# Optimization experiments

Hardware: AMD Instinct MI355X
Metric: run time of the kernel (lower is better)

Reference implementation:

```python
import jax, jax.numpy as jnp
import numpy as np

H, W, NF, K, MD, ND, NDM, MLP_H = 128, 128, 8, 9, 16, 8, 8, 64
NPIX = H * W
RADIUS = int((K ** 0.5 - 1) // 2)


def _compute_neighbors_adjusted(height, width, radius):
    # Faithful port of LocalResiduals._compute_neighbors_adjusted (setup-time only).
    Kn = (2 * radius + 1) ** 2
    base = np.stack(np.meshgrid(np.arange(-radius, radius + 1),
                                np.arange(-radius, radius + 1), indexing='ij'),
                    axis=-1).reshape(-1, 2)
    neighbors = np.empty((height * width, Kn), dtype=np.int64)
    for i in range(height):
        for j in range(width):
            off = base.copy()
            ni = i + off[:, 0]
            nj = j + off[:, 1]
            valid = (ni >= 0) & (ni < height) & (nj >= 0) & (nj < width)
            valid_inds = list(ni[valid] * width + nj[valid])
            expansion = 1
            while len(valid_inds) < Kn:
                r_ext = radius + expansion
                ext = np.stack(np.meshgrid(np.arange(-r_ext, r_ext + 1),
                                           np.arange(-r_ext, r_ext + 1), indexing='ij'),
                               axis=-1).reshape(-1, 2)
                seen = set(map(tuple, off.tolist()))
                ext_new = np.array([t for t in map(tuple, ext.tolist()) if t not in seen],
                                   dtype=np.int64)
                off = np.concatenate([off, ext_new], axis=0)
                ni_e = i + ext_new[:, 0]
                nj_e = j + ext_new[:, 1]
                valid_e = (ni_e >= 0) & (ni_e < height) & (nj_e >= 0) & (nj_e < width)
                valid_inds += list(ni_e[valid_e] * width + nj_e[valid_e])
                expansion += 1
            neighbors[i * width + j] = np.array(valid_inds[:Kn], dtype=np.int64)
    return neighbors


def setup_inputs() -> dict:
    key = jax.random.key(0)
    ks = jax.random.split(key, 8)
    B = 16
    y_in = jax.random.normal(ks[0], (B, NF, H, W), dtype=jnp.float32)
    noise = jax.random.normal(ks[1], (B, ND, NPIX), dtype=jnp.float32)
    noise2 = jax.random.normal(ks[2], (B, NPIX, NDM), dtype=jnp.float32)
    n_in = NF + ND
    # xavier-uniform-like init for weight_map
    bound = float(np.sqrt(6.0 / (MD + n_in)))
    weight_map = jax.random.uniform(ks[3], (NPIX, K, MD, n_in), dtype=jnp.float32,
                                    minval=-bound, maxval=bound)
    d0 = MD + NDM
    w1 = jax.random.normal(ks[4], (MLP_H, d0), dtype=jnp.float32) / np.sqrt(d0)
    b1 = jnp.zeros((MLP_H,), dtype=jnp.float32)
    w2 = jax.random.normal(ks[5], (NF, MLP_H), dtype=jnp.float32) / np.sqrt(MLP_H)
    b2 = jnp.zeros((NF,), dtype=jnp.float32)
    neighbor_idx = jnp.asarray(_compute_neighbors_adjusted(H, W, RADIUS))  # (NPIX, K)
    return {"y_in": y_in, "noise": noise, "noise2": noise2,
            "weight_map": weight_map, "w1": w1, "b1": b1, "w2": w2, "b2": b2,
            "neighbor_idx": neighbor_idx}


def reference(y_in, noise, noise2, weight_map, w1, b1, w2, b2, neighbor_idx):
    B = y_in.shape[0]
    y_flat = y_in.reshape(B, NF, NPIX)
    y_with_noise = jnp.concatenate([y_flat, noise], axis=1)        # (B, NF+ND, NPIX)
    feats = jnp.transpose(y_with_noise, (0, 2, 1))                  # (B, NPIX, NF+ND)
    gather_y = feats[:, neighbor_idx, :]                            # (B, NPIX, K, NF+ND)
    # per-pixel distinct weight contraction
    intermediate = jnp.einsum('bpkn,pkmn->bpm', gather_y, weight_map)  # (B, NPIX, MD)
    mlp_in = jnp.concatenate([intermediate, noise2], axis=-1)      # (B, NPIX, MD+NDM)
    h = jax.nn.relu(jnp.einsum('bpd,hd->bph', mlp_in, w1) + b1)
    out = jnp.einsum('bph,fh->bpf', h, w2) + b2                    # (B, NPIX, NF)
    out = jnp.transpose(out, (0, 2, 1)).reshape(B, NF, H, W)
    return out
```

## Files before the change

### kernel.cpp

```cpp
#include <hip/hip_runtime.h>

#define NPIX 16384

typedef _Float16 f16;
typedef __attribute__((ext_vector_type(8))) _Float16 half8;
typedef __attribute__((ext_vector_type(8))) unsigned short ushort8;
typedef __attribute__((ext_vector_type(4))) float f32x4;

__device__ inline half8 cvt8_nt(const float* __restrict__ p) {
  f32x4 a = __builtin_nontemporal_load((const f32x4*)p);
  f32x4 b = __builtin_nontemporal_load((const f32x4*)p + 1);
  half8 r;
  r[0] = (f16)a.x; r[1] = (f16)a.y; r[2] = (f16)a.z; r[3] = (f16)a.w;
  r[4] = (f16)b.x; r[5] = (f16)b.y; r[6] = (f16)b.z; r[7] = (f16)b.w;
  return r;
}
__device__ inline half8 cvt8(const float* __restrict__ p) {
  f32x4 a = *(const f32x4*)p;
  f32x4 b = *(const f32x4*)(p + 4);
  half8 r;
  r[0] = (f16)a.x; r[1] = (f16)a.y; r[2] = (f16)a.z; r[3] = (f16)a.w;
  r[4] = (f16)b.x; r[5] = (f16)b.y; r[6] = (f16)b.z; r[7] = (f16)b.w;
  return r;
}

__global__ __launch_bounds__(256) void pack_feats(
    const float* __restrict__ y,
    const float* __restrict__ nz,
    f16* __restrict__ out)
{
  __shared__ f16 tile[64][258];
  const int p0 = blockIdx.x << 6;
  const int t = threadIdx.x;
  const int lane16 = t & 15;
  const int pl0 = t >> 4;
  #pragma unroll
  for (int g = 0; g < 16; ++g) {
    const int plane = g * 16 + pl0;
    const int b = plane >> 4, n = plane & 15;
    const float* src = (n < 8) ? (y + (b * 8 + n) * NPIX)
                               : (nz + (b * 8 + (n - 8)) * NPIX);
    f32x4 v = __builtin_nontemporal_load((const f32x4*)(src + p0 + lane16 * 4));
    tile[lane16 * 4 + 0][plane] = (f16)v.x;
    tile[lane16 * 4 + 1][plane] = (f16)v.y;
    tile[lane16 * 4 + 2][plane] = (f16)v.z;
    tile[lane16 * 4 + 3][plane] = (f16)v.w;
  }
  __syncthreads();
  #pragma unroll
  for (int it = 0; it < 8; ++it) {
    const int idx = it * 256 + t;
    const int px = idx >> 5;
    const int c = idx & 31;
    ushort8 v = *(const ushort8*)&tile[px][c * 8];
    *(ushort8*)(out + (p0 + px) * 256 + c * 8) = v;
  }
}

__global__ __launch_bounds__(256, 4) void lr_einsum(
    const f16*  __restrict__ feats,
    const float* __restrict__ wmap,
    const int*  __restrict__ nidx,
    f16* __restrict__ inter)
{
  const int t = threadIdx.x;
  const int wv = t >> 6;
  const int l = t & 63;
  const int col = l & 15;
  const int q = l >> 4;

  const int bid = blockIdx.x;
  const int p = ((((bid & 7) << 9) + (bid >> 3)) << 2) + wv;

  const int n0 = (q & 1) * 8;
  const int kh = q >> 1;

  const int ps = __builtin_amdgcn_readfirstlane(p);
  int nb[9];
  #pragma unroll
  for (int k = 0; k < 9; ++k)
    nb[k] = __builtin_amdgcn_readfirstlane(nidx[ps * 9 + k]);

  half8 af[5], bfr[5];
  #pragma unroll
  for (int c = 0; c < 4; ++c) {
    const int k = 2 * c + kh;
    af[c]  = *(const half8*)(feats + nb[k] * 256 + col * 16 + n0);
    bfr[c] = cvt8_nt(wmap + ((ps * 9 + k) * 16 + col) * 16 + n0);
  }
  af[4]  = (half8){0, 0, 0, 0, 0, 0, 0, 0};
  bfr[4] = (half8){0, 0, 0, 0, 0, 0, 0, 0};
  if (q < 2) {
    af[4]  = *(const half8*)(feats + nb[8] * 256 + col * 16 + n0);
    bfr[4] = cvt8_nt(wmap + ((ps * 9 + 8) * 16 + col) * 16 + n0);
  }
  f32x4 acc = {0.f, 0.f, 0.f, 0.f};
  #pragma unroll
  for (int c = 0; c < 5; ++c)
    acc = __builtin_amdgcn_mfma_f32_16x16x32_f16(af[c], bfr[c], acc, 0, 0, 0);

  #pragma unroll
  for (int r = 0; r < 4; ++r)
    inter[p * 256 + (q * 4 + r) * 16 + col] = (f16)acc[r];
}

__global__ __launch_bounds__(512) void lr_mlp(
    const f16*  __restrict__ inter,
    const float* __restrict__ noise2,
    const float* __restrict__ w1,
    const float* __restrict__ b1,
    const float* __restrict__ w2,
    const float* __restrict__ b2,
    float* __restrict__ outp)
{
  __shared__ f16 lds_h[8][16 * 72];
  __shared__ __align__(16) float stage[128 * 36];

  const int t = threadIdx.x;
  const int wv = t >> 6;
  const int l = t & 63;
  const int col = l & 15;
  const int q = l >> 4;

  const int bid = blockIdx.x;
  const int slab = ((bid & 7) << 6) + (bid >> 3);
  const int p0 = slab << 5;
  const int pw0 = p0 + wv * 4;

  f16* lh = lds_h[wv];

  half8 w1f[4];
  float b1f[4];
  #pragma unroll
  for (int jc = 0; jc < 4; ++jc) {
    w1f[jc] = (half8){0, 0, 0, 0, 0, 0, 0, 0};
    if (q < 3) w1f[jc] = cvt8(w1 + (jc * 16 + col) * 24 + q * 8);
    b1f[jc] = b1[jc * 16 + col];
  }
  half8 w2f[2] = {{0, 0, 0, 0, 0, 0, 0, 0}, {0, 0, 0, 0, 0, 0, 0, 0}};
  float b2f = 0.f;
  if (col < 8) {
    w2f[0] = cvt8(w2 + col * 64 + q * 8);
    w2f[1] = cvt8(w2 + col * 64 + 32 + q * 8);
    b2f = b2[col];
  }
  half8 n2f[4];
  #pragma unroll
  for (int px = 0; px < 4; ++px) {
    n2f[px] = (half8){0, 0, 0, 0, 0, 0, 0, 0};
    if (q == 2) n2f[px] = cvt8(noise2 + (col * NPIX + pw0 + px) * 8);
  }

  const f32x4 zero4 = {0.f, 0.f, 0.f, 0.f};

  #pragma unroll
  for (int px = 0; px < 4; ++px) {
    const int p = pw0 + px;

    half8 amlp = n2f[px];
    if (q < 2) amlp = *(const half8*)(inter + p * 256 + col * 16 + q * 8);

    #pragma unroll
    for (int jc = 0; jc < 4; ++jc) {
      f32x4 h4 = __builtin_amdgcn_mfma_f32_16x16x32_f16(amlp, w1f[jc], zero4, 0, 0, 0);
      #pragma unroll
      for (int r = 0; r < 4; ++r) {
        float hv = fmaxf(h4[r] + b1f[jc], 0.f);
        lh[(q * 4 + r) * 72 + jc * 16 + col] = (f16)hv;
      }
    }

    f32x4 oacc = zero4;
    #pragma unroll
    for (int c2 = 0; c2 < 2; ++c2) {
      half8 a2 = *(const half8*)(lh + col * 72 + c2 * 32 + q * 8);
      oacc = __builtin_amdgcn_mfma_f32_16x16x32_f16(a2, w2f[c2], oacc, 0, 0, 0);
    }
    if (col < 8) {
      const int pxl = wv * 4 + px;
      #pragma unroll
      for (int r = 0; r < 4; ++r) {
        const int row = q * 32 + r * 8 + col;
        stage[row * 36 + pxl] = oacc[r] + b2f;
      }
    }
  }

  __syncthreads();

  #pragma unroll
  for (int rr = 0; rr < 2; ++rr) {
    const int idx = rr * 512 + t;
    const int row = idx >> 3;
    const int c8 = idx & 7;
    f32x4 v = *(const f32x4*)&stage[row * 36 + c8 * 4];
    *(f32x4*)(outp + row * NPIX + p0 + c8 * 4) = v;
  }
}

extern "C" void kernel_launch(void* const* d_in, const int* in_sizes, int n_in,
                              void* d_out, int out_size, void* d_ws, size_t ws_size,
                              hipStream_t stream) {
  const float* y    = (const float*)d_in[0];
  const float* nz   = (const float*)d_in[1];
  const float* nz2  = (const float*)d_in[2];
  const float* wmap = (const float*)d_in[3];
  const float* w1   = (const float*)d_in[4];
  const float* b1   = (const float*)d_in[5];
  const float* w2   = (const float*)d_in[6];
  const float* b2   = (const float*)d_in[7];
  const int* nidx   = (const int*)d_in[8];
  float* outp = (float*)d_out;
  f16* feats = (f16*)d_ws;
  f16* inter = (f16*)((char*)d_ws + (size_t)NPIX * 256 * 2);

  hipLaunchKernelGGL(pack_feats, dim3(NPIX / 64), dim3(256), 0, stream,
                     y, nz, feats);
  hipLaunchKernelGGL(lr_einsum, dim3(NPIX / 4), dim3(256), 0, stream,
                     feats, wmap, nidx, inter);
  hipLaunchKernelGGL(lr_mlp, dim3(NPIX / 32), dim3(512), 0, stream,
                     inter, nz2, w1, b1, w2, b2, outp);
}
```

Measured before the change: 250.6 us.

## Fuse per-pixel einsum and MLP kernels, prepack noise2 in pack kernel

Merges the einsum and MLP kernels into one kernel, so the intermediate stays in LDS instead of going through global memory. The noise2 conversion and transpose to f16 moves into the pack kernel, which writes a pixel-major layout so the fused kernel can do one vector load per lane. The cost is that each block now loads w1 and w2 fragments for only 4 pixels instead of 32. Output stores also become narrow 8-byte writes per row.

```diff
diff --git a/kernel.cpp b/kernel.cpp
--- a/kernel.cpp
+++ b/kernel.cpp
@@ -6,6 +6,7 @@
 typedef __attribute__((ext_vector_type(8))) _Float16 half8;
 typedef __attribute__((ext_vector_type(8))) unsigned short ushort8;
 typedef __attribute__((ext_vector_type(4))) float f32x4;
+typedef __attribute__((ext_vector_type(2))) float f32x2;
 
 __device__ inline half8 cvt8_nt(const float* __restrict__ p) {
   f32x4 a = __builtin_nontemporal_load((const f32x4*)p);
@@ -27,7 +28,9 @@
 __global__ __launch_bounds__(256) void pack_feats(
     const float* __restrict__ y,
     const float* __restrict__ nz,
-    f16* __restrict__ out)
+    const float* __restrict__ nz2,
+    f16* __restrict__ outf,
+    f16* __restrict__ n2p)
 {
   __shared__ f16 tile[64][258];
   const int p0 = blockIdx.x << 6;
@@ -46,6 +49,14 @@
     tile[lane16 * 4 + 2][plane] = (f16)v.z;
     tile[lane16 * 4 + 3][plane] = (f16)v.w;
   }
+  #pragma unroll
+  for (int it = 0; it < 4; ++it) {
+    const int pair = it * 256 + t;
+    const int b = pair >> 6;
+    const int pl = pair & 63;
+    half8 v = cvt8_nt(nz2 + (size_t)(b * NPIX + p0 + pl) * 8);
+    *(half8*)(n2p + (p0 + pl) * 128 + b * 8) = v;
+  }
   __syncthreads();
   #pragma unroll
   for (int it = 0; it < 8; ++it) {
@@ -53,68 +64,24 @@
     const int px = idx >> 5;
     const int c = idx & 31;
     ushort8 v = *(const ushort8*)&tile[px][c * 8];
-    *(ushort8*)(out + (p0 + px) * 256 + c * 8) = v;
-  }
-}
-
-__global__ __launch_bounds__(256, 4) void lr_einsum(
+    *(ushort8*)(outf + (p0 + px) * 256 + c * 8) = v;
+  }
+}
+
+__global__ __launch_bounds__(256, 4) void lr_fused(
     const f16*  __restrict__ feats,
+    const f16*  __restrict__ n2p,
     const float* __restrict__ wmap,
     const int*  __restrict__ nidx,
-    f16* __restrict__ inter)
-{
-  const int t = threadIdx.x;
-  const int wv = t >> 6;
-  const int l = t & 63;
-  const int col = l & 15;
-  const int q = l >> 4;
-
-  const int bid = blockIdx.x;
-  const int p = ((((bid & 7) << 9) + (bid >> 3)) << 2) + wv;
-
-  const int n0 = (q & 1) * 8;
-  const int kh = q >> 1;
-
-  const int ps = __builtin_amdgcn_readfirstlane(p);
-  int nb[9];
-  #pragma unroll
-  for (int k = 0; k < 9; ++k)
-    nb[k] = __builtin_amdgcn_readfirstlane(nidx[ps * 9 + k]);
-
-  half8 af[5], bfr[5];
-  #pragma unroll
-  for (int c = 0; c < 4; ++c) {
-    const int k = 2 * c + kh;
-    af[c]  = *(const half8*)(feats + nb[k] * 256 + col * 16 + n0);
-    bfr[c] = cvt8_nt(wmap + ((ps * 9 + k) * 16 + col) * 16 + n0);
-  }
-  af[4]  = (half8){0, 0, 0, 0, 0, 0, 0, 0};
-  bfr[4] = (half8){0, 0, 0, 0, 0, 0, 0, 0};
-  if (q < 2) {
-    af[4]  = *(const half8*)(feats + nb[8] * 256 + col * 16 + n0);
-    bfr[4] = cvt8_nt(wmap + ((ps * 9 + 8) * 16 + col) * 16 + n0);
-  }
-  f32x4 acc = {0.f, 0.f, 0.f, 0.f};
-  #pragma unroll
-  for (int c = 0; c < 5; ++c)
-    acc = __builtin_amdgcn_mfma_f32_16x16x32_f16(af[c], bfr[c], acc, 0, 0, 0);
-
-  #pragma unroll
-  for (int r = 0; r < 4; ++r)
-    inter[p * 256 + (q * 4 + r) * 16 + col] = (f16)acc[r];
-}
-
-__global__ __launch_bounds__(512) void lr_mlp(
-    const f16*  __restrict__ inter,
-    const float* __restrict__ noise2,
     const float* __restrict__ w1,
     const float* __restrict__ b1,
     const float* __restrict__ w2,
     const float* __restrict__ b2,
     float* __restrict__ outp)
 {
-  __shared__ f16 lds_h[8][16 * 72];
-  __shared__ __align__(16) float stage[128 * 36];
+  __shared__ f16 tbuf[4][256];
+  __shared__ f16 lds_h[4][16 * 72];
+  __shared__ __align__(16) float stage[128][4];
 
   const int t = threadIdx.x;
   const int wv = t >> 6;
@@ -123,11 +90,40 @@
   const int q = l >> 4;
 
   const int bid = blockIdx.x;
-  const int slab = ((bid & 7) << 6) + (bid >> 3);
-  const int p0 = slab << 5;
-  const int pw0 = p0 + wv * 4;
-
-  f16* lh = lds_h[wv];
+  const int p0 = ((((bid & 7) << 9) + (bid >> 3)) << 2);
+  const int p = p0 + wv;
+
+  const int n0 = (q & 1) * 8;
+  const int kh = q >> 1;
+
+  const int ps = __builtin_amdgcn_readfirstlane(p);
+  int nb[9];
+  #pragma unroll
+  for (int k = 0; k < 9; ++k)
+    nb[k] = __builtin_amdgcn_readfirstlane(nidx[ps * 9 + k]);
+
+  half8 af[5], bfr[5];
+  #pragma unroll
+  for (int c = 0; c < 4; ++c) {
+    const int k = 2 * c + kh;
+    af[c]  = *(const half8*)(feats + nb[k] * 256 + col * 16 + n0);
+    bfr[c] = cvt8_nt(wmap + ((ps * 9 + k) * 16 + col) * 16 + n0);
+  }
+  af[4]  = (half8){0, 0, 0, 0, 0, 0, 0, 0};
+  bfr[4] = (half8){0, 0, 0, 0, 0, 0, 0, 0};
+  if (q < 2) {
+    af[4]  = *(const half8*)(feats + nb[8] * 256 + col * 16 + n0);
+    bfr[4] = cvt8_nt(wmap + ((ps * 9 + 8) * 16 + col) * 16 + n0);
+  }
+  f32x4 acc = {0.f, 0.f, 0.f, 0.f};
+  #pragma unroll
+  for (int c = 0; c < 5; ++c)
+    acc = __builtin_amdgcn_mfma_f32_16x16x32_f16(af[c], bfr[c], acc, 0, 0, 0);
+
+  f16* tb = tbuf[wv];
+  #pragma unroll
+  for (int r = 0; r < 4; ++r)
+    tb[(q * 4 + r) * 16 + col] = (f16)acc[r];
 
   half8 w1f[4];
   float b1f[4];
@@ -144,57 +140,46 @@
     w2f[1] = cvt8(w2 + col * 64 + 32 + q * 8);
     b2f = b2[col];
   }
-  half8 n2f[4];
-  #pragma unroll
-  for (int px = 0; px < 4; ++px) {
-    n2f[px] = (half8){0, 0, 0, 0, 0, 0, 0, 0};
-    if (q == 2) n2f[px] = cvt8(noise2 + (col * NPIX + pw0 + px) * 8);
-  }
+  half8 n2v = (half8){0, 0, 0, 0, 0, 0, 0, 0};
+  if (q == 2) n2v = *(const half8*)(n2p + p * 128 + col * 8);
 
   const f32x4 zero4 = {0.f, 0.f, 0.f, 0.f};
 
-  #pragma unroll
-  for (int px = 0; px < 4; ++px) {
-    const int p = pw0 + px;
-
-    half8 amlp = n2f[px];
-    if (q < 2) amlp = *(const half8*)(inter + p * 256 + col * 16 + q * 8);
-
+  half8 amlp = n2v;
+  if (q < 2) amlp = *(const half8*)(tb + col * 16 + q * 8);
+
+  f16* lh = lds_h[wv];
+  #pragma unroll
+  for (int jc = 0; jc < 4; ++jc) {
+    f32x4 h4 = __builtin_amdgcn_mfma_f32_16x16x32_f16(amlp, w1f[jc], zero4, 0, 0, 0);
     #pragma unroll
-    for (int jc = 0; jc < 4; ++jc) {
-      f32x4 h4 = __builtin_amdgcn_mfma_f32_16x16x32_f16(amlp, w1f[jc], zero4, 0, 0, 0);
-      #pragma unroll
-      for (int r = 0; r < 4; ++r) {
-        float hv = fmaxf(h4[r] + b1f[jc], 0.f);
-        lh[(q * 4 + r) * 72 + jc * 16 + col] = (f16)hv;
-      }
+    for (int r = 0; r < 4; ++r) {
+      float hv = fmaxf(h4[r] + b1f[jc], 0.f);
+      lh[(q * 4 + r) * 72 + jc * 16 + col] = (f16)hv;
     }
-
-    f32x4 oacc = zero4;
+  }
+
+  f32x4 oacc = zero4;
+  #pragma unroll
+  for (int c2 = 0; c2 < 2; ++c2) {
+    half8 a2 = *(const half8*)(lh + col * 72 + c2 * 32 + q * 8);
+    oacc = __builtin_amdgcn_mfma_f32_16x16x32_f16(a2, w2f[c2], oacc, 0, 0, 0);
+  }
+  if (col < 8) {
     #pragma unroll
-    for (int c2 = 0; c2 < 2; ++c2) {
-      half8 a2 = *(const half8*)(lh + col * 72 + c2 * 32 + q * 8);
-      oacc = __builtin_amdgcn_mfma_f32_16x16x32_f16(a2, w2f[c2], oacc, 0, 0, 0);
+    for (int r = 0; r < 4; ++r) {
+      const int row = q * 32 + r * 8 + col;
+      stage[row][wv] = oacc[r] + b2f;
     }
-    if (col < 8) {
-      const int pxl = wv * 4 + px;
-      #pragma unroll
-      for (int r = 0; r < 4; ++r) {
-        const int row = q * 32 + r * 8 + col;
-        stage[row * 36 + pxl] = oacc[r] + b2f;
-      }
-    }
   }
 
   __syncthreads();
 
-  #pragma unroll
-  for (int rr = 0; rr < 2; ++rr) {
-    const int idx = rr * 512 + t;
-    const int row = idx >> 3;
-    const int c8 = idx & 7;
-    f32x4 v = *(const f32x4*)&stage[row * 36 + c8 * 4];
-    *(f32x4*)(outp + row * NPIX + p0 + c8 * 4) = v;
+  {
+    const int row = t >> 1;
+    const int h2 = (t & 1) * 2;
+    f32x2 v = *(const f32x2*)&stage[row][h2];
+    *(f32x2*)(outp + row * NPIX + p0 + h2) = v;
   }
 }
 
@@ -212,12 +197,10 @@
   const int* nidx   = (const int*)d_in[8];
   float* outp = (float*)d_out;
   f16* feats = (f16*)d_ws;
-  f16* inter = (f16*)((char*)d_ws + (size_t)NPIX * 256 * 2);
+  f16* n2p   = (f16*)((char*)d_ws + (size_t)NPIX * 256 * 2);
 
   hipLaunchKernelGGL(pack_feats, dim3(NPIX / 64), dim3(256), 0, stream,
-                     y, nz, feats);
-  hipLaunchKernelGGL(lr_einsum, dim3(NPIX / 4), dim3(256), 0, stream,
-                     feats, wmap, nidx, inter);
-  hipLaunchKernelGGL(lr_mlp, dim3(NPIX / 32), dim3(512), 0, stream,
-                     inter, nz2, w1, b1, w2, b2, outp);
-}
+                     y, nz, nz2, feats, n2p);
+  hipLaunchKernelGGL(lr_fused, dim3(NPIX / 4), dim3(256), 0, stream,
+                     feats, n2p, wmap, nidx, w1, b1, w2, b2, outp);
+}
```

Measured after the change: 248.7 us. Within noise of the previous version (-0.8%).
